# Optimization experiments

Hardware: AMD Instinct MI355X
Metric: run time of the kernel (lower is better)

Reference implementation:

```python
import jax, jax.numpy as jnp
import numpy as np

D_MODEL = 256
N_HEADS = 8
N_LEVELS = 3
N_POINTS = 4
HEAD_DIM = D_MODEL // N_HEADS
SPATIAL_SHAPES = [(80, 80), (40, 40), (20, 20)]
B = 16
LEN_Q = 300
N_TOTAL = sum(h * w for h, w in SPATIAL_SHAPES)  # 8400
N_LP = N_LEVELS * N_POINTS


def setup_inputs() -> dict:
    key = jax.random.key(0)
    ks = jax.random.split(key, 8)
    s = 0.02
    return {
        "query": jax.random.normal(ks[0], (B, LEN_Q, D_MODEL), jnp.float32),
        "reference_points": jax.random.uniform(ks[1], (B, LEN_Q, N_LEVELS, 2), jnp.float32),
        "input_flatten": jax.random.normal(ks[2], (B, N_TOTAL, D_MODEL), jnp.float32),
        "W_off": jax.random.normal(ks[3], (D_MODEL, N_HEADS * N_LP * 2), jnp.float32) * s,
        "b_off": jnp.zeros((N_HEADS * N_LP * 2,), jnp.float32),
        "W_attn": jax.random.normal(ks[4], (D_MODEL, N_HEADS * N_LP), jnp.float32) * s,
        "b_attn": jnp.zeros((N_HEADS * N_LP,), jnp.float32),
        "W_val": jax.random.normal(ks[5], (D_MODEL, D_MODEL), jnp.float32) * s,
        "b_val": jnp.zeros((D_MODEL,), jnp.float32),
        "W_out": jax.random.normal(ks[6], (D_MODEL, D_MODEL), jnp.float32) * s,
        "b_out": jnp.zeros((D_MODEL,), jnp.float32),
    }


def _ms_deform_core(value, sampling_locations, attention_weights):
    # value: (B, n_heads, head_dim, N_total); locations: (B, Lq, H, L, P, 2) in [0,1]
    Bq, Lq = sampling_locations.shape[0], sampling_locations.shape[1]
    BN = Bq * N_HEADS
    grids = 2.0 * sampling_locations - 1.0
    starts = np.cumsum([0] + [h * w for h, w in SPATIAL_SHAPES])
    sampled_levels = []
    for lid, (H, W) in enumerate(SPATIAL_SHAPES):
        val_l = value[..., starts[lid]:starts[lid + 1]]                    # (B,H,hd,HW)
        val_flat = val_l.reshape(BN, HEAD_DIM, H * W).transpose(0, 2, 1)   # (BN,HW,hd)
        g = grids[:, :, :, lid].transpose(0, 2, 1, 3, 4).reshape(BN, Lq, N_POINTS, 2)
        ix = ((g[..., 0] + 1.0) * W - 1.0) / 2.0
        iy = ((g[..., 1] + 1.0) * H - 1.0) / 2.0
        ix0 = jnp.floor(ix).astype(jnp.int32)
        iy0 = jnp.floor(iy).astype(jnp.int32)
        ix1 = ix0 + 1
        iy1 = iy0 + 1
        fx = (ix - ix0.astype(ix.dtype))[..., None]
        fy = (iy - iy0.astype(iy.dtype))[..., None]

        def corner(iyc, ixc):
            valid = ((ixc >= 0) & (ixc < W) & (iyc >= 0) & (iyc < H)).astype(val_flat.dtype)
            idx = (jnp.clip(iyc, 0, H - 1) * W + jnp.clip(ixc, 0, W - 1))
            idx = idx.reshape(BN, Lq * N_POINTS, 1)
            v = jnp.take_along_axis(val_flat, idx, axis=1)
            return v.reshape(BN, Lq, N_POINTS, HEAD_DIM) * valid[..., None]

        v00 = corner(iy0, ix0)
        v01 = corner(iy0, ix1)
        v10 = corner(iy1, ix0)
        v11 = corner(iy1, ix1)
        sampled = ((1 - fx) * (1 - fy)) * v00 + (fx * (1 - fy)) * v01 \
                + ((1 - fx) * fy) * v10 + (fx * fy) * v11
        sampled_levels.append(sampled.transpose(0, 3, 1, 2))               # (BN,hd,Lq,P)
    sv = jnp.stack(sampled_levels, axis=-2).reshape(BN, HEAD_DIM, Lq, N_LP)
    a = attention_weights.transpose(0, 2, 1, 3).reshape(BN, 1, Lq, N_LP)
    out = jnp.sum(sv * a, axis=-1)                                         # (BN,hd,Lq)
    return out.reshape(Bq, D_MODEL, Lq).transpose(0, 2, 1)                 # (B,Lq,D)


def reference(query, reference_points, input_flatten,
              W_off, b_off, W_attn, b_attn, W_val, b_val, W_out, b_out):
    Bq, Lq = query.shape[0], query.shape[1]
    value = input_flatten @ W_val + b_val
    value = value.reshape(Bq, -1, N_HEADS, HEAD_DIM).transpose(0, 2, 3, 1)  # (B,H,hd,N)
    off = (query @ W_off + b_off).reshape(Bq, Lq, N_HEADS, N_LEVELS, N_POINTS, 2)
    attn = jax.nn.softmax((query @ W_attn + b_attn).reshape(Bq, Lq, N_HEADS, N_LP), axis=-1)
    # offset normalizer is (W,H) per level (x first)
    norm = jnp.array([[w, h] for h, w in SPATIAL_SHAPES], jnp.float32)
    loc = reference_points[:, :, None, :, None, :] + off / norm[None, None, None, :, None, :]
    out = _ms_deform_core(value, loc, attn)
    return out @ W_out + b_out
```

## Files before the change

kernel.cpp:

```cpp
#include <hip/hip_runtime.h>
#include <hip/hip_bf16.h>

#define DM 256
#define NH 8
#define HD 32
#define NLV 3
#define NPT 4
#define NLP 12
#define BB 16
#define LQ 300
#define NT 8400
#define MROWS (BB * NT)
#define QROWS (BB * LQ)
#define KP2 72
#define VB (MROWS / 64)

typedef __bf16 bf16x8 __attribute__((ext_vector_type(8)));
typedef float  f32x16 __attribute__((ext_vector_type(16)));

__global__ void k_wt(const float* __restrict__ W_val,
                     const float* __restrict__ W_off,
                     const float* __restrict__ W_attn,
                     const float* __restrict__ W_out,
                     __hip_bfloat16* __restrict__ Wf,
                     __hip_bfloat16* __restrict__ Wf2,
                     __hip_bfloat16* __restrict__ Wf3)
{
    const int n = blockIdx.x;
    const int k = threadIdx.x;
    if (n < 256) {
        Wf[(size_t)(k >> 3) * 2048 + n * 8 + (k & 7)] =
            __float2bfloat16(W_val[(size_t)k * 256 + n]);
    } else if (n < 544) {
        const int n2 = n - 256;
        float v = (n2 < 192) ? W_off[(size_t)k * 192 + n2]
                             : W_attn[(size_t)k * 96 + (n2 - 192)];
        Wf2[(size_t)(k >> 3) * 2304 + n2 * 8 + (k & 7)] = __float2bfloat16(v);
    } else {
        const int n3 = n - 544;
        Wf3[(size_t)(k >> 3) * 2048 + n3 * 8 + (k & 7)] =
            __float2bfloat16(W_out[(size_t)k * 256 + n3]);
    }
}

__global__ __launch_bounds__(256) void k_mm1(
    const float* __restrict__ A,
    const __hip_bfloat16* __restrict__ Wf,
    const float* __restrict__ bval,
    __hip_bfloat16* __restrict__ V,
    const float* __restrict__ Q,
    const __hip_bfloat16* __restrict__ Wf2,
    const float* __restrict__ boff,
    const float* __restrict__ battn,
    float* __restrict__ off_out,
    float* __restrict__ attn_out)
{
    __shared__ __hip_bfloat16 As[2][64 * KP2];

    const int t    = threadIdx.x;
    const int wave = t >> 6;
    const int lane = t & 63;
    const int lm   = lane & 31;
    const int kh   = lane >> 5;
    const int lk   = kh * 8;

    if (blockIdx.x < VB) {
        const int m0  = blockIdx.x * 64;
        const int ar2 = t >> 2;
        const int ak2 = (t & 3) * 16;

        f32x16 acc[2][2];
#pragma unroll
        for (int i = 0; i < 2; i++)
#pragma unroll
            for (int j = 0; j < 2; j++)
#pragma unroll
                for (int e = 0; e < 16; e++) acc[i][j][e] = 0.f;

        const __hip_bfloat16* wf0 = Wf + (size_t)(wave * 64 + lm) * 8 + kh * 2048;

        {
            const float* ap = A + (size_t)(m0 + ar2) * 256 + ak2;
            float4 a0 = *(const float4*)ap;
            float4 a1 = *(const float4*)(ap + 4);
            float4 a2 = *(const float4*)(ap + 8);
            float4 a3 = *(const float4*)(ap + 12);
            union { __hip_bfloat162 h2[4]; bf16x8 v; } u0, u1;
            u0.h2[0] = __float22bfloat162_rn(make_float2(a0.x, a0.y));
            u0.h2[1] = __float22bfloat162_rn(make_float2(a0.z, a0.w));
            u0.h2[2] = __float22bfloat162_rn(make_float2(a1.x, a1.y));
            u0.h2[3] = __float22bfloat162_rn(make_float2(a1.z, a1.w));
            u1.h2[0] = __float22bfloat162_rn(make_float2(a2.x, a2.y));
            u1.h2[1] = __float22bfloat162_rn(make_float2(a2.z, a2.w));
            u1.h2[2] = __float22bfloat162_rn(make_float2(a3.x, a3.y));
            u1.h2[3] = __float22bfloat162_rn(make_float2(a3.z, a3.w));
            *(bf16x8*)(&As[0][ar2 * KP2 + ak2])     = u0.v;
            *(bf16x8*)(&As[0][ar2 * KP2 + ak2 + 8]) = u1.v;
        }
        __syncthreads();

#pragma unroll
        for (int it = 0; it < 4; ++it) {
            const int buf = it & 1;
            float4 na0, na1, na2, na3;
            if (it < 3) {
                const float* ap = A + (size_t)(m0 + ar2) * 256 + (it + 1) * 64 + ak2;
                na0 = *(const float4*)ap;
                na1 = *(const float4*)(ap + 4);
                na2 = *(const float4*)(ap + 8);
                na3 = *(const float4*)(ap + 12);
            }
#pragma unroll
            for (int ks = 0; ks < 4; ++ks) {
                const int g = it * 4 + ks;
                bf16x8 af0 = *(const bf16x8*)(&As[buf][(lm)      * KP2 + ks * 16 + lk]);
                bf16x8 af1 = *(const bf16x8*)(&As[buf][(32 + lm) * KP2 + ks * 16 + lk]);
                bf16x8 b0  = *(const bf16x8*)(wf0 + (size_t)g * 4096);
                bf16x8 b1  = *(const bf16x8*)(wf0 + (size_t)g * 4096 + 256);
                acc[0][0] = __builtin_amdgcn_mfma_f32_32x32x16_bf16(af0, b0, acc[0][0], 0, 0, 0);
                acc[0][1] = __builtin_amdgcn_mfma_f32_32x32x16_bf16(af0, b1, acc[0][1], 0, 0, 0);
                acc[1][0] = __builtin_amdgcn_mfma_f32_32x32x16_bf16(af1, b0, acc[1][0], 0, 0, 0);
                acc[1][1] = __builtin_amdgcn_mfma_f32_32x32x16_bf16(af1, b1, acc[1][1], 0, 0, 0);
            }
            if (it < 3) {
                union { __hip_bfloat162 h2[4]; bf16x8 v; } u0, u1;
                u0.h2[0] = __float22bfloat162_rn(make_float2(na0.x, na0.y));
                u0.h2[1] = __float22bfloat162_rn(make_float2(na0.z, na0.w));
                u0.h2[2] = __float22bfloat162_rn(make_float2(na1.x, na1.y));
                u0.h2[3] = __float22bfloat162_rn(make_float2(na1.z, na1.w));
                u1.h2[0] = __float22bfloat162_rn(make_float2(na2.x, na2.y));
                u1.h2[1] = __float22bfloat162_rn(make_float2(na2.z, na2.w));
                u1.h2[2] = __float22bfloat162_rn(make_float2(na3.x, na3.y));
                u1.h2[3] = __float22bfloat162_rn(make_float2(na3.z, na3.w));
                *(bf16x8*)(&As[buf ^ 1][ar2 * KP2 + ak2])     = u0.v;
                *(bf16x8*)(&As[buf ^ 1][ar2 * KP2 + ak2 + 8]) = u1.v;
                __syncthreads();
            }
        }

        const int bb  = m0 / NT;
        const int bnd = (bb + 1) * NT;
#pragma unroll
        for (int i = 0; i < 2; i++) {
#pragma unroll
            for (int j = 0; j < 2; j++) {
                const int n  = wave * 64 + j * 32 + lm;
                const float bn = bval[n];
                const int h  = n >> 5;
                const int d  = n & 31;
#pragma unroll
                for (int r = 0; r < 16; r++) {
                    int rl = (r & 3) + 8 * (r >> 2) + 4 * kh;
                    int m  = m0 + i * 32 + rl;
                    int b  = bb + ((m >= bnd) ? 1 : 0);
                    int pos = m - b * NT;
                    V[((size_t)(b * NH + h) * NT + pos) * HD + d] =
                        __float2bfloat16(acc[i][j][r] + bn);
                }
            }
        }
    } else {
        const int m0 = (blockIdx.x - VB) * 32;
        const int ar = t >> 3;
        const int ak = (t & 7) * 8;

        f32x16 acc[3];
#pragma unroll
        for (int j = 0; j < 3; j++)
#pragma unroll
            for (int e = 0; e < 16; e++) acc[j][e] = 0.f;

        const __hip_bfloat16* wf0 = Wf2 + (size_t)(wave * 96 + lm) * 8 + kh * 2304;

        {
            const float* ap = Q + (size_t)(m0 + ar) * 256 + ak;
            float4 a0 = *(const float4*)ap;
            float4 a1 = *(const float4*)(ap + 4);
            union { __hip_bfloat162 h2[4]; bf16x8 v; } ua;
            ua.h2[0] = __float22bfloat162_rn(make_float2(a0.x, a0.y));
            ua.h2[1] = __float22bfloat162_rn(make_float2(a0.z, a0.w));
            ua.h2[2] = __float22bfloat162_rn(make_float2(a1.x, a1.y));
            ua.h2[3] = __float22bfloat162_rn(make_float2(a1.z, a1.w));
            *(bf16x8*)(&As[0][ar * KP2 + ak]) = ua.v;
        }
        __syncthreads();

#pragma unroll
        for (int it = 0; it < 4; ++it) {
            const int buf = it & 1;
            float4 na0, na1;
            if (it < 3) {
                const float* ap = Q + (size_t)(m0 + ar) * 256 + (it + 1) * 64 + ak;
                na0 = *(const float4*)ap;
                na1 = *(const float4*)(ap + 4);
            }
#pragma unroll
            for (int ks = 0; ks < 4; ++ks) {
                const int g = it * 4 + ks;
                bf16x8 af = *(const bf16x8*)(&As[buf][lm * KP2 + ks * 16 + lk]);
                if (wave < 3) {
#pragma unroll
                    for (int j = 0; j < 3; j++) {
                        bf16x8 bf = *(const bf16x8*)(wf0 + (size_t)g * 4608 + j * 256);
                        acc[j] = __builtin_amdgcn_mfma_f32_32x32x16_bf16(af, bf, acc[j], 0, 0, 0);
                    }
                }
            }
            if (it < 3) {
                union { __hip_bfloat162 h2[4]; bf16x8 v; } ua;
                ua.h2[0] = __float22bfloat162_rn(make_float2(na0.x, na0.y));
                ua.h2[1] = __float22bfloat162_rn(make_float2(na0.z, na0.w));
                ua.h2[2] = __float22bfloat162_rn(make_float2(na1.x, na1.y));
                ua.h2[3] = __float22bfloat162_rn(make_float2(na1.z, na1.w));
                *(bf16x8*)(&As[buf ^ 1][ar * KP2 + ak]) = ua.v;
                __syncthreads();
            }
        }

        if (wave < 3) {
#pragma unroll
            for (int j = 0; j < 3; j++) {
                const int n = wave * 96 + j * 32 + lm;
                const float bias_ = (n < 192) ? boff[n] : battn[n - 192];
#pragma unroll
                for (int r = 0; r < 16; r++) {
                    int rl = (r & 3) + 8 * (r >> 2) + 4 * kh;
                    int m  = m0 + rl;
                    float v = acc[j][r] + bias_;
                    if (n < 192) off_out[(size_t)m * 192 + n] = v;
                    else         attn_out[(size_t)m * 96 + (n - 192)] = v;
                }
            }
        }
    }
}

__global__ __launch_bounds__(256) void k_sample(
    const float* __restrict__ off_raw,
    const float* __restrict__ attn_raw,
    const float* __restrict__ refp,
    const __hip_bfloat16* __restrict__ V,
    __hip_bfloat16* __restrict__ sampled)
{
    const int t = threadIdx.x;

    const int bid  = blockIdx.x;
    const int xcd  = bid & 7;
    const int slot = bid >> 3;
    const int hi   = (slot >= 75) ? 1 : 0;
    const int b    = xcd + (hi << 3);
    const int q0   = (slot - hi * 75) * 4;
    const int bq0  = b * LQ + q0;

    __shared__ float aw[4][96];
    __shared__ float wc[4][96][4];
    __shared__ int   ic[4][96][4];

    if (t < 32) {
        const int q = t >> 3, h = t & 7;
        const float* arp = attn_raw + (size_t)(bq0 + q) * 96 + h * 12;
        float4 x0 = *(const float4*)arp;
        float4 x1 = *(const float4*)(arp + 4);
        float4 x2 = *(const float4*)(arp + 8);
        float v[12] = {x0.x, x0.y, x0.z, x0.w,
                       x1.x, x1.y, x1.z, x1.w,
                       x2.x, x2.y, x2.z, x2.w};
        float mx = -1e30f;
#pragma unroll
        for (int i = 0; i < 12; i++) mx = fmaxf(mx, v[i]);
        float s = 0.f;
#pragma unroll
        for (int i = 0; i < 12; i++) { v[i] = expf(v[i] - mx); s += v[i]; }
        float inv = 1.f / s;
#pragma unroll
        for (int i = 0; i < 12; i++) aw[q][h * 12 + i] = v[i] * inv;
    }
    __syncthreads();

#pragma unroll
    for (int i = t; i < 384; i += 256) {
        const int q  = i / 96;
        const int s  = i - q * 96;
        const int bq = bq0 + q;
        const float dims[3]  = {80.f, 40.f, 20.f};
        const int startsl[3] = {0, 6400, 8000};
        const int idiml[3]   = {80, 40, 20};
        int h = s / 12, lp = s - h * 12, l = lp >> 2, p = lp & 3;
        float2 o2 = *(const float2*)(off_raw + (size_t)bq * 192 + ((h * 3 + l) * 4 + p) * 2);
        float2 r2 = *(const float2*)(refp + (size_t)bq * 6 + l * 2);
        float D  = dims[l];
        float ix = (r2.x + o2.x / D) * D - 0.5f;
        float iy = (r2.y + o2.y / D) * D - 0.5f;
        const int Dl = idiml[l];
        const int st = startsl[l];

        float fix = floorf(ix), fiy = floorf(iy);
        int ix0 = (int)fix, iy0 = (int)fiy;
        int ix1 = ix0 + 1, iy1 = iy0 + 1;
        float fx = ix - fix, fy = iy - fiy;

        float mx0 = (ix0 >= 0 && ix0 < Dl) ? 1.f : 0.f;
        float mx1 = (ix1 >= 0 && ix1 < Dl) ? 1.f : 0.f;
        float my0 = (iy0 >= 0 && iy0 < Dl) ? 1.f : 0.f;
        float my1 = (iy1 >= 0 && iy1 < Dl) ? 1.f : 0.f;

        int cx0 = min(max(ix0, 0), Dl - 1);
        int cx1 = min(max(ix1, 0), Dl - 1);
        int cy0 = min(max(iy0, 0), Dl - 1);
        int cy1 = min(max(iy1, 0), Dl - 1);

        float a = aw[q][s];
        wc[q][s][0] = (1.f - fx) * (1.f - fy) * mx0 * my0 * a;
        wc[q][s][1] = fx * (1.f - fy) * mx1 * my0 * a;
        wc[q][s][2] = (1.f - fx) * fy * mx0 * my1 * a;
        wc[q][s][3] = fx * fy * mx1 * my1 * a;
        ic[q][s][0] = (st + cy0 * Dl + cx0) * HD;
        ic[q][s][1] = (st + cy0 * Dl + cx1) * HD;
        ic[q][s][2] = (st + cy1 * Dl + cx0) * HD;
        ic[q][s][3] = (st + cy1 * Dl + cx1) * HD;
    }
    __syncthreads();

    const int q  = t >> 6;
    const int u  = t & 63;
    const int h  = u >> 3;
    const int dt = (u & 7) * 4;
    const int bq = bq0 + q;
    const __hip_bfloat16* vb = V + (size_t)(b * NH + h) * NT * HD + dt;

    float a0 = 0.f, a1 = 0.f, a2 = 0.f, a3 = 0.f;
#pragma unroll
    for (int lp = 0; lp < 12; lp++) {
        const int s = h * 12 + lp;
        float4 w4 = *(const float4*)(&wc[q][s][0]);
        int4   i4 = *(const int4*)(&ic[q][s][0]);
        union { uint2 u2; __hip_bfloat162 h2[2]; } c0, c1, c2, c3;
        c0.u2 = *(const uint2*)(vb + i4.x);
        c1.u2 = *(const uint2*)(vb + i4.y);
        c2.u2 = *(const uint2*)(vb + i4.z);
        c3.u2 = *(const uint2*)(vb + i4.w);
        float2 f0a = __bfloat1622float2(c0.h2[0]), f0b = __bfloat1622float2(c0.h2[1]);
        float2 f1a = __bfloat1622float2(c1.h2[0]), f1b = __bfloat1622float2(c1.h2[1]);
        float2 f2a = __bfloat1622float2(c2.h2[0]), f2b = __bfloat1622float2(c2.h2[1]);
        float2 f3a = __bfloat1622float2(c3.h2[0]), f3b = __bfloat1622float2(c3.h2[1]);
        a0 = fmaf(w4.x, f0a.x, fmaf(w4.y, f1a.x, fmaf(w4.z, f2a.x, fmaf(w4.w, f3a.x, a0))));
        a1 = fmaf(w4.x, f0a.y, fmaf(w4.y, f1a.y, fmaf(w4.z, f2a.y, fmaf(w4.w, f3a.y, a1))));
        a2 = fmaf(w4.x, f0b.x, fmaf(w4.y, f1b.x, fmaf(w4.z, f2b.x, fmaf(w4.w, f3b.x, a2))));
        a3 = fmaf(w4.x, f0b.y, fmaf(w4.y, f1b.y, fmaf(w4.z, f2b.y, fmaf(w4.w, f3b.y, a3))));
    }
    union { ushort4 s4; __hip_bfloat162 h2[2]; } ou;
    ou.h2[0] = __float22bfloat162_rn(make_float2(a0, a1));
    ou.h2[1] = __float22bfloat162_rn(make_float2(a2, a3));
    *(ushort4*)(sampled + (size_t)bq * 256 + h * 32 + dt) = ou.s4;
}

__global__ __launch_bounds__(256) void k_outproj(
    const __hip_bfloat16* __restrict__ A,
    const __hip_bfloat16* __restrict__ Wf3,
    const float* __restrict__ bias,
    float* __restrict__ out)
{
    __shared__ __hip_bfloat16 As[2][32 * KP2];

    const int t    = threadIdx.x;
    const int m0   = blockIdx.x * 32;
    const int wave = t >> 6;
    const int lane = t & 63;
    const int lm   = lane & 31;
    const int kh   = lane >> 5;
    const int lk   = kh * 8;
    const int ar   = t >> 3;
    const int ak   = (t & 7) * 8;

    f32x16 acc[2];
#pragma unroll
    for (int j = 0; j < 2; j++)
#pragma unroll
        for (int e = 0; e < 16; e++) acc[j][e] = 0.f;

    const __hip_bfloat16* wf0 = Wf3 + (size_t)(wave * 64 + lm) * 8 + kh * 2048;

    *(bf16x8*)(&As[0][ar * KP2 + ak]) =
        *(const bf16x8*)(A + (size_t)(m0 + ar) * 256 + ak);
    __syncthreads();

#pragma unroll
    for (int it = 0; it < 4; ++it) {
        const int buf = it & 1;
        bf16x8 na;
        if (it < 3)
            na = *(const bf16x8*)(A + (size_t)(m0 + ar) * 256 + (it + 1) * 64 + ak);
#pragma unroll
        for (int ks = 0; ks < 4; ++ks) {
            const int g = it * 4 + ks;
            bf16x8 af = *(const bf16x8*)(&As[buf][lm * KP2 + ks * 16 + lk]);
            bf16x8 b0 = *(const bf16x8*)(wf0 + (size_t)g * 4096);
            bf16x8 b1 = *(const bf16x8*)(wf0 + (size_t)g * 4096 + 256);
            acc[0] = __builtin_amdgcn_mfma_f32_32x32x16_bf16(af, b0, acc[0], 0, 0, 0);
            acc[1] = __builtin_amdgcn_mfma_f32_32x32x16_bf16(af, b1, acc[1], 0, 0, 0);
        }
        if (it < 3) {
            *(bf16x8*)(&As[buf ^ 1][ar * KP2 + ak]) = na;
            __syncthreads();
        }
    }

#pragma unroll
    for (int j = 0; j < 2; j++) {
        const int n = wave * 64 + j * 32 + lm;
        const float bn = bias[n];
#pragma unroll
        for (int r = 0; r < 16; r++) {
            int rl = (r & 3) + 8 * (r >> 2) + 4 * kh;
            int m  = m0 + rl;
            out[(size_t)m * 256 + n] = acc[j][r] + bn;
        }
    }
}

extern "C" void kernel_launch(void* const* d_in, const int* in_sizes, int n_in,
                              void* d_out, int out_size, void* d_ws, size_t ws_size,
                              hipStream_t stream) {
    const float* query  = (const float*)d_in[0];
    const float* refp   = (const float*)d_in[1];
    const float* inputf = (const float*)d_in[2];
    const float* W_off  = (const float*)d_in[3];
    const float* b_off  = (const float*)d_in[4];
    const float* W_attn = (const float*)d_in[5];
    const float* b_attn = (const float*)d_in[6];
    const float* W_val  = (const float*)d_in[7];
    const float* b_val  = (const float*)d_in[8];
    const float* W_out  = (const float*)d_in[9];
    const float* b_out  = (const float*)d_in[10];
    float* out = (float*)d_out;

    char* ws = (char*)d_ws;
    __hip_bfloat16* value   = (__hip_bfloat16*)ws;
    float* off_raw          = (float*)(ws + 68812800);
    float* attn_raw         = (float*)(ws + 72499200);
    __hip_bfloat16* sampled = (__hip_bfloat16*)(ws + 74342400);
    __hip_bfloat16* Wf      = (__hip_bfloat16*)(ws + 76800000);
    __hip_bfloat16* Wf2     = (__hip_bfloat16*)(ws + 76931072);
    __hip_bfloat16* Wf3     = (__hip_bfloat16*)(ws + 77078528);

    k_wt<<<800, 256, 0, stream>>>(W_val, W_off, W_attn, W_out, Wf, Wf2, Wf3);
    k_mm1<<<VB + QROWS / 32, 256, 0, stream>>>(
        inputf, Wf, b_val, value, query, Wf2, b_off, b_attn, off_raw, attn_raw);
    k_sample<<<1200, 256, 0, stream>>>(off_raw, attn_raw, refp, value, sampled);
    k_outproj<<<QROWS / 32, 256, 0, stream>>>(sampled, Wf3, b_out, out);
}
```

Before: 261.9 us.

## Stage full K=256 A tile in LDS upfront instead of double-buffered K chunks

```diff
diff --git a/kernel.cpp b/kernel.cpp
--- a/kernel.cpp
+++ b/kernel.cpp
@@ -12,7 +12,7 @@
 #define NT 8400
 #define MROWS (BB * NT)
 #define QROWS (BB * LQ)
-#define KP2 72
+#define KP3 264
 #define VB (MROWS / 64)
 
 typedef __bf16 bf16x8 __attribute__((ext_vector_type(8)));
@@ -55,7 +55,7 @@
     float* __restrict__ off_out,
     float* __restrict__ attn_out)
 {
-    __shared__ __hip_bfloat16 As[2][64 * KP2];
+    __shared__ __hip_bfloat16 As[64 * KP3];
 
     const int t    = threadIdx.x;
     const int wave = t >> 6;
@@ -69,6 +69,30 @@
         const int ar2 = t >> 2;
         const int ak2 = (t & 3) * 16;
 
+        const float* ap = A + (size_t)(m0 + ar2) * 256 + ak2;
+        float4 r[16];
+#pragma unroll
+        for (int it = 0; it < 4; ++it)
+#pragma unroll
+            for (int c = 0; c < 4; ++c)
+                r[it * 4 + c] = *(const float4*)(ap + it * 64 + c * 4);
+
+#pragma unroll
+        for (int it = 0; it < 4; ++it) {
+            union { __hip_bfloat162 h2[4]; bf16x8 v; } u0, u1;
+            u0.h2[0] = __float22bfloat162_rn(make_float2(r[it*4+0].x, r[it*4+0].y));
+            u0.h2[1] = __float22bfloat162_rn(make_float2(r[it*4+0].z, r[it*4+0].w));
+            u0.h2[2] = __float22bfloat162_rn(make_float2(r[it*4+1].x, r[it*4+1].y));
+            u0.h2[3] = __float22bfloat162_rn(make_float2(r[it*4+1].z, r[it*4+1].w));
+            u1.h2[0] = __float22bfloat162_rn(make_float2(r[it*4+2].x, r[it*4+2].y));
+            u1.h2[1] = __float22bfloat162_rn(make_float2(r[it*4+2].z, r[it*4+2].w));
+            u1.h2[2] = __float22bfloat162_rn(make_float2(r[it*4+3].x, r[it*4+3].y));
+            u1.h2[3] = __float22bfloat162_rn(make_float2(r[it*4+3].z, r[it*4+3].w));
+            *(bf16x8*)(&As[ar2 * KP3 + it * 64 + ak2])     = u0.v;
+            *(bf16x8*)(&As[ar2 * KP3 + it * 64 + ak2 + 8]) = u1.v;
+        }
+        __syncthreads();
+
         f32x16 acc[2][2];
 #pragma unroll
         for (int i = 0; i < 2; i++)
@@ -79,63 +103,16 @@
 
         const __hip_bfloat16* wf0 = Wf + (size_t)(wave * 64 + lm) * 8 + kh * 2048;
 
-        {
-            const float* ap = A + (size_t)(m0 + ar2) * 256 + ak2;
-            float4 a0 = *(const float4*)ap;
-            float4 a1 = *(const float4*)(ap + 4);
-            float4 a2 = *(const float4*)(ap + 8);
-            float4 a3 = *(const float4*)(ap + 12);
-            union { __hip_bfloat162 h2[4]; bf16x8 v; } u0, u1;
-            u0.h2[0] = __float22bfloat162_rn(make_float2(a0.x, a0.y));
-            u0.h2[1] = __float22bfloat162_rn(make_float2(a0.z, a0.w));
-            u0.h2[2] = __float22bfloat162_rn(make_float2(a1.x, a1.y));
-            u0.h2[3] = __float22bfloat162_rn(make_float2(a1.z, a1.w));
-            u1.h2[0] = __float22bfloat162_rn(make_float2(a2.x, a2.y));
-            u1.h2[1] = __float22bfloat162_rn(make_float2(a2.z, a2.w));
-            u1.h2[2] = __float22bfloat162_rn(make_float2(a3.x, a3.y));
-            u1.h2[3] = __float22bfloat162_rn(make_float2(a3.z, a3.w));
-            *(bf16x8*)(&As[0][ar2 * KP2 + ak2])     = u0.v;
-            *(bf16x8*)(&As[0][ar2 * KP2 + ak2 + 8]) = u1.v;
-        }
-        __syncthreads();
-
-#pragma unroll
-        for (int it = 0; it < 4; ++it) {
-            const int buf = it & 1;
-            float4 na0, na1, na2, na3;
-            if (it < 3) {
-                const float* ap = A + (size_t)(m0 + ar2) * 256 + (it + 1) * 64 + ak2;
-                na0 = *(const float4*)ap;
-                na1 = *(const float4*)(ap + 4);
-                na2 = *(const float4*)(ap + 8);
-                na3 = *(const float4*)(ap + 12);
-            }
-#pragma unroll
-            for (int ks = 0; ks < 4; ++ks) {
-                const int g = it * 4 + ks;
-                bf16x8 af0 = *(const bf16x8*)(&As[buf][(lm)      * KP2 + ks * 16 + lk]);
-                bf16x8 af1 = *(const bf16x8*)(&As[buf][(32 + lm) * KP2 + ks * 16 + lk]);
-                bf16x8 b0  = *(const bf16x8*)(wf0 + (size_t)g * 4096);
-                bf16x8 b1  = *(const bf16x8*)(wf0 + (size_t)g * 4096 + 256);
-                acc[0][0] = __builtin_amdgcn_mfma_f32_32x32x16_bf16(af0, b0, acc[0][0], 0, 0, 0);
-                acc[0][1] = __builtin_amdgcn_mfma_f32_32x32x16_bf16(af0, b1, acc[0][1], 0, 0, 0);
-                acc[1][0] = __builtin_amdgcn_mfma_f32_32x32x16_bf16(af1, b0, acc[1][0], 0, 0, 0);
-                acc[1][1] = __builtin_amdgcn_mfma_f32_32x32x16_bf16(af1, b1, acc[1][1], 0, 0, 0);
-            }
-            if (it < 3) {
-                union { __hip_bfloat162 h2[4]; bf16x8 v; } u0, u1;
-                u0.h2[0] = __float22bfloat162_rn(make_float2(na0.x, na0.y));
-                u0.h2[1] = __float22bfloat162_rn(make_float2(na0.z, na0.w));
-                u0.h2[2] = __float22bfloat162_rn(make_float2(na1.x, na1.y));
-                u0.h2[3] = __float22bfloat162_rn(make_float2(na1.z, na1.w));
-                u1.h2[0] = __float22bfloat162_rn(make_float2(na2.x, na2.y));
-                u1.h2[1] = __float22bfloat162_rn(make_float2(na2.z, na2.w));
-                u1.h2[2] = __float22bfloat162_rn(make_float2(na3.x, na3.y));
-                u1.h2[3] = __float22bfloat162_rn(make_float2(na3.z, na3.w));
-                *(bf16x8*)(&As[buf ^ 1][ar2 * KP2 + ak2])     = u0.v;
-                *(bf16x8*)(&As[buf ^ 1][ar2 * KP2 + ak2 + 8]) = u1.v;
-                __syncthreads();
-            }
+#pragma unroll
+        for (int ks = 0; ks < 16; ++ks) {
+            bf16x8 af0 = *(const bf16x8*)(&As[(lm)      * KP3 + ks * 16 + lk]);
+            bf16x8 af1 = *(const bf16x8*)(&As[(32 + lm) * KP3 + ks * 16 + lk]);
+            bf16x8 b0  = *(const bf16x8*)(wf0 + (size_t)ks * 4096);
+            bf16x8 b1  = *(const bf16x8*)(wf0 + (size_t)ks * 4096 + 256);
+            acc[0][0] = __builtin_amdgcn_mfma_f32_32x32x16_bf16(af0, b0, acc[0][0], 0, 0, 0);
+            acc[0][1] = __builtin_amdgcn_mfma_f32_32x32x16_bf16(af0, b1, acc[0][1], 0, 0, 0);
+            acc[1][0] = __builtin_amdgcn_mfma_f32_32x32x16_bf16(af1, b0, acc[1][0], 0, 0, 0);
+            acc[1][1] = __builtin_amdgcn_mfma_f32_32x32x16_bf16(af1, b1, acc[1][1], 0, 0, 0);
         }
 
         const int bb  = m0 / NT;
@@ -149,13 +126,13 @@
                 const int h  = n >> 5;
                 const int d  = n & 31;
 #pragma unroll
-                for (int r = 0; r < 16; r++) {
-                    int rl = (r & 3) + 8 * (r >> 2) + 4 * kh;
+                for (int r2 = 0; r2 < 16; r2++) {
+                    int rl = (r2 & 3) + 8 * (r2 >> 2) + 4 * kh;
                     int m  = m0 + i * 32 + rl;
                     int b  = bb + ((m >= bnd) ? 1 : 0);
                     int pos = m - b * NT;
                     V[((size_t)(b * NH + h) * NT + pos) * HD + d] =
-                        __float2bfloat16(acc[i][j][r] + bn);
+                        __float2bfloat16(acc[i][j][r2] + bn);
                 }
             }
         }
@@ -164,6 +141,24 @@
         const int ar = t >> 3;
         const int ak = (t & 7) * 8;
 
+        const float* ap = Q + (size_t)(m0 + ar) * 256 + ak;
+        float4 r[8];
+#pragma unroll
+        for (int it = 0; it < 4; ++it) {
+            r[it * 2 + 0] = *(const float4*)(ap + it * 64);
+            r[it * 2 + 1] = *(const float4*)(ap + it * 64 + 4);
+        }
+#pragma unroll
+        for (int it = 0; it < 4; ++it) {
+            union { __hip_bfloat162 h2[4]; bf16x8 v; } ua;
+            ua.h2[0] = __float22bfloat162_rn(make_float2(r[it*2+0].x, r[it*2+0].y));
+            ua.h2[1] = __float22bfloat162_rn(make_float2(r[it*2+0].z, r[it*2+0].w));
+            ua.h2[2] = __float22bfloat162_rn(make_float2(r[it*2+1].x, r[it*2+1].y));
+            ua.h2[3] = __float22bfloat162_rn(make_float2(r[it*2+1].z, r[it*2+1].w));
+            *(bf16x8*)(&As[ar * KP3 + it * 64 + ak]) = ua.v;
+        }
+        __syncthreads();
+
         f32x16 acc[3];
 #pragma unroll
         for (int j = 0; j < 3; j++)
@@ -172,61 +167,25 @@
 
         const __hip_bfloat16* wf0 = Wf2 + (size_t)(wave * 96 + lm) * 8 + kh * 2304;
 
-        {
-            const float* ap = Q + (size_t)(m0 + ar) * 256 + ak;
-            float4 a0 = *(const float4*)ap;
-            float4 a1 = *(const float4*)(ap + 4);
-            union { __hip_bfloat162 h2[4]; bf16x8 v; } ua;
-            ua.h2[0] = __float22bfloat162_rn(make_float2(a0.x, a0.y));
-            ua.h2[1] = __float22bfloat162_rn(make_float2(a0.z, a0.w));
-            ua.h2[2] = __float22bfloat162_rn(make_float2(a1.x, a1.y));
-            ua.h2[3] = __float22bfloat162_rn(make_float2(a1.z, a1.w));
-            *(bf16x8*)(&As[0][ar * KP2 + ak]) = ua.v;
-        }
-        __syncthreads();
-
-#pragma unroll
-        for (int it = 0; it < 4; ++it) {
-            const int buf = it & 1;
-            float4 na0, na1;
-            if (it < 3) {
-                const float* ap = Q + (size_t)(m0 + ar) * 256 + (it + 1) * 64 + ak;
-                na0 = *(const float4*)ap;
-                na1 = *(const float4*)(ap + 4);
-            }
-#pragma unroll
-            for (int ks = 0; ks < 4; ++ks) {
-                const int g = it * 4 + ks;
-                bf16x8 af = *(const bf16x8*)(&As[buf][lm * KP2 + ks * 16 + lk]);
-                if (wave < 3) {
-#pragma unroll
-                    for (int j = 0; j < 3; j++) {
-                        bf16x8 bf = *(const bf16x8*)(wf0 + (size_t)g * 4608 + j * 256);
-                        acc[j] = __builtin_amdgcn_mfma_f32_32x32x16_bf16(af, bf, acc[j], 0, 0, 0);
-                    }
+        if (wave < 3) {
+#pragma unroll
+            for (int ks = 0; ks < 16; ++ks) {
+                bf16x8 af = *(const bf16x8*)(&As[lm * KP3 + ks * 16 + lk]);
+#pragma unroll
+                for (int j = 0; j < 3; j++) {
+                    bf16x8 bf = *(const bf16x8*)(wf0 + (size_t)ks * 4608 + j * 256);
+                    acc[j] = __builtin_amdgcn_mfma_f32_32x32x16_bf16(af, bf, acc[j], 0, 0, 0);
                 }
             }
-            if (it < 3) {
-                union { __hip_bfloat162 h2[4]; bf16x8 v; } ua;
-                ua.h2[0] = __float22bfloat162_rn(make_float2(na0.x, na0.y));
-                ua.h2[1] = __float22bfloat162_rn(make_float2(na0.z, na0.w));
-                ua.h2[2] = __float22bfloat162_rn(make_float2(na1.x, na1.y));
-                ua.h2[3] = __float22bfloat162_rn(make_float2(na1.z, na1.w));
-                *(bf16x8*)(&As[buf ^ 1][ar * KP2 + ak]) = ua.v;
-                __syncthreads();
-            }
-        }
-
-        if (wave < 3) {
 #pragma unroll
             for (int j = 0; j < 3; j++) {
                 const int n = wave * 96 + j * 32 + lm;
                 const float bias_ = (n < 192) ? boff[n] : battn[n - 192];
 #pragma unroll
-                for (int r = 0; r < 16; r++) {
-                    int rl = (r & 3) + 8 * (r >> 2) + 4 * kh;
+                for (int r2 = 0; r2 < 16; r2++) {
+                    int rl = (r2 & 3) + 8 * (r2 >> 2) + 4 * kh;
                     int m  = m0 + rl;
-                    float v = acc[j][r] + bias_;
+                    float v = acc[j][r2] + bias_;
                     if (n < 192) off_out[(size_t)m * 192 + n] = v;
                     else         attn_out[(size_t)m * 96 + (n - 192)] = v;
                 }
@@ -360,7 +319,7 @@
     const float* __restrict__ bias,
     float* __restrict__ out)
 {
-    __shared__ __hip_bfloat16 As[2][32 * KP2];
+    __shared__ __hip_bfloat16 As[32 * KP3];
 
     const int t    = threadIdx.x;
     const int m0   = blockIdx.x * 32;
@@ -372,6 +331,16 @@
     const int ar   = t >> 3;
     const int ak   = (t & 7) * 8;
 
+    const __hip_bfloat16* apg = A + (size_t)(m0 + ar) * 256 + ak;
+    bf16x8 rr[4];
+#pragma unroll
+    for (int it = 0; it < 4; ++it)
+        rr[it] = *(const bf16x8*)(apg + it * 64);
+#pragma unroll
+    for (int it = 0; it < 4; ++it)
+        *(bf16x8*)(&As[ar * KP3 + it * 64 + ak]) = rr[it];
+    __syncthreads();
+
     f32x16 acc[2];
 #pragma unroll
     for (int j = 0; j < 2; j++)
@@ -380,29 +349,13 @@
 
     const __hip_bfloat16* wf0 = Wf3 + (size_t)(wave * 64 + lm) * 8 + kh * 2048;
 
-    *(bf16x8*)(&As[0][ar * KP2 + ak]) =
-        *(const bf16x8*)(A + (size_t)(m0 + ar) * 256 + ak);
-    __syncthreads();
-
-#pragma unroll
-    for (int it = 0; it < 4; ++it) {
-        const int buf = it & 1;
-        bf16x8 na;
-        if (it < 3)
-            na = *(const bf16x8*)(A + (size_t)(m0 + ar) * 256 + (it + 1) * 64 + ak);
-#pragma unroll
-        for (int ks = 0; ks < 4; ++ks) {
-            const int g = it * 4 + ks;
-            bf16x8 af = *(const bf16x8*)(&As[buf][lm * KP2 + ks * 16 + lk]);
-            bf16x8 b0 = *(const bf16x8*)(wf0 + (size_t)g * 4096);
-            bf16x8 b1 = *(const bf16x8*)(wf0 + (size_t)g * 4096 + 256);
-            acc[0] = __builtin_amdgcn_mfma_f32_32x32x16_bf16(af, b0, acc[0], 0, 0, 0);
-            acc[1] = __builtin_amdgcn_mfma_f32_32x32x16_bf16(af, b1, acc[1], 0, 0, 0);
-        }
-        if (it < 3) {
-            *(bf16x8*)(&As[buf ^ 1][ar * KP2 + ak]) = na;
-            __syncthreads();
-        }
+#pragma unroll
+    for (int ks = 0; ks < 16; ++ks) {
+        bf16x8 af = *(const bf16x8*)(&As[lm * KP3 + ks * 16 + lk]);
+        bf16x8 b0 = *(const bf16x8*)(wf0 + (size_t)ks * 4096);
+        bf16x8 b1 = *(const bf16x8*)(wf0 + (size_t)ks * 4096 + 256);
+        acc[0] = __builtin_amdgcn_mfma_f32_32x32x16_bf16(af, b0, acc[0], 0, 0, 0);
+        acc[1] = __builtin_amdgcn_mfma_f32_32x32x16_bf16(af, b1, acc[1], 0, 0, 0);
     }
 
 #pragma unroll
@@ -410,10 +363,10 @@
         const int n = wave * 64 + j * 32 + lm;
         const float bn = bias[n];
 #pragma unroll
-        for (int r = 0; r < 16; r++) {
-            int rl = (r & 3) + 8 * (r >> 2) + 4 * kh;
+        for (int r2 = 0; r2 < 16; r2++) {
+            int rl = (r2 & 3) + 8 * (r2 >> 2) + 4 * kh;
             int m  = m0 + rl;
-            out[(size_t)m * 256 + n] = acc[j][r] + bn;
+            out[(size_t)m * 256 + n] = acc[j][r2] + bn;
         }
     }
 }
```

Result: no change. 264.9 us (+1.1%).
